# Kernel optimization log

Hardware: AMD Instinct MI355X
Metric: run time of the kernel (lower is better)

The kernel has to match this reference:

```python
import jax, jax.numpy as jnp
import numpy as np

N = 100000   # nodes
E = 800000   # edges
IN = 256     # input feature dim
H = 4        # heads per layer
D = 32       # per-head hidden dim (num_hidden)
SLOPE = 0.2  # leaky_relu negative slope


def setup_inputs() -> dict:
    key = jax.random.key(0)
    ks = jax.random.split(key, 8)
    s = 0.1  # weight scale for numerical stability
    x = jax.random.normal(ks[0], (N, IN), jnp.float32)
    edge_index = jax.random.randint(ks[1], (2, E), 0, N, dtype=jnp.int32)
    W0 = jax.random.normal(ks[2], (IN, H * D), jnp.float32) * s
    al0 = jax.random.normal(ks[3], (H, D), jnp.float32) * s
    ar0 = jax.random.normal(ks[4], (H, D), jnp.float32) * s
    W1 = jax.random.normal(ks[5], (H * D, H * D), jnp.float32) * s
    al1 = jax.random.normal(ks[6], (H, D), jnp.float32) * s
    ar1 = jax.random.normal(ks[7], (H, D), jnp.float32) * s
    return {"x": x, "edge_index": edge_index, "W0": W0, "al0": al0,
            "ar0": ar0, "W1": W1, "al1": al1, "ar1": ar1}


def _gat_layer(h, W, al, ar, src, dst, residual):
    """One GATConv: project, edge attention, dst-wise softmax, scatter-agg."""
    n = h.shape[0]
    feat = (h @ W).reshape(n, H, D)              # [N,H,D]
    el = jnp.einsum('nhd,hd->nh', feat, al)      # [N,H]
    er = jnp.einsum('nhd,hd->nh', feat, ar)      # [N,H]
    e = jax.nn.leaky_relu(el[src] + er[dst], SLOPE)   # raw scores [E,H]
    # edge softmax grouped by destination node (numerically stable)
    emax = jax.ops.segment_max(e, dst, num_segments=n)   # [N,H]
    eexp = jnp.exp(e - emax[dst])                          # [E,H]
    denom = jax.ops.segment_sum(eexp, dst, num_segments=n)  # [N,H]
    a = eexp / denom[dst]                                  # attention [E,H]
    msg = feat[src] * a[:, :, None]                        # [E,H,D]
    rst = jax.ops.segment_sum(msg, dst, num_segments=n)    # [N,H,D]
    if residual:
        rst = rst + h.reshape(n, H, D)  # identity residual (dims match)
    rst = jax.nn.elu(rst)               # activation
    return rst, a, e


def reference(x, edge_index, W0, al0, ar0, W1, al1, ar1):
    src, dst = edge_index[0], edge_index[1]
    # layer 0: no residual
    h1, a0, e0 = _gat_layer(x, W0, al0, ar0, src, dst, residual=False)
    atten0 = e0.mean(axis=-1)  # e_gat.flatten(1).mean(-1) -> [E]
    # layer 1: residual
    h2, a1, e1 = _gat_layer(h1.reshape(N, H * D), W1, al1, ar1, src, dst,
                            residual=True)
    atten1 = e1.mean(axis=-1)
    temp = h2.reshape(N, H * D)          # flattened node embeddings
    heads = tuple(h2[:, i] for i in range(H))  # per-head [N,D]
    return (temp,) + heads + (e1, atten0, atten1)
```

## Files before the change

### kernel.cpp

```cpp
#include <hip/hip_runtime.h>
#include <hip/hip_bf16.h>


typedef _Float16 f16;
typedef _Float16 f16x2 __attribute__((ext_vector_type(2)));
typedef _Float16 f16x8 __attribute__((ext_vector_type(8)));
typedef float f32x4 __attribute__((ext_vector_type(4)));

__global__ void wsplit2(const float* __restrict__ W0, const float* __restrict__ W1,
                        f16* __restrict__ Wth0, f16* __restrict__ Wtl0,
                        f16* __restrict__ Wth1, f16* __restrict__ Wtl1) {
    int i = blockIdx.x * blockDim.x + threadIdx.x;
    if (i < 256 * 128) {
        int k = i >> 7, c = i & 127;
        float v = W0[i];
        f16 h = (f16)v;
        Wth0[(size_t)c * 256 + k] = h;
        Wtl0[(size_t)c * 256 + k] = (f16)(v - (float)h);
    } else if (i < 256 * 128 + 128 * 128) {
        int j = i - 256 * 128;
        int k = j >> 7, c = j & 127;
        float v = W1[j];
        f16 h = (f16)v;
        Wth1[(size_t)c * 128 + k] = h;
        Wtl1[(size_t)c * 128 + k] = (f16)(v - (float)h);
    }
}

template <int AFP16>
__global__ __launch_bounds__(256, 2) void gemm_mfma(
        const void* __restrict__ Xv, const f16* __restrict__ Wth,
        const f16* __restrict__ Wtl, f16* __restrict__ Y16,
        const float* __restrict__ al, const float* __restrict__ ar,
        float* __restrict__ el_out, float* __restrict__ er_out,
        int nrows, int K) {
    constexpr int STR = 40;
    __shared__ f16 ash[128 * STR];
    __shared__ f16 asl[AFP16 ? 2 : 128 * STR];
    __shared__ f16 bsh[128 * STR];
    __shared__ f16 bsl[128 * STR];
    const int t    = threadIdx.x;
    const int wave = t >> 6;
    const int lane = t & 63;
    const int lr   = lane & 15;
    const int kg   = lane >> 4;
    const int row0 = blockIdx.x * 128;

    const int sr  = t >> 1;
    const int sko = (t & 1) * 16;
    const int ps  = ((sr & 7) << 4) | (sr >> 3);
    int gr = row0 + sr; if (gr >= nrows) gr = nrows - 1;

    f32x4 acc[2][8];
    #pragma unroll
    for (int i = 0; i < 2; ++i)
        #pragma unroll
        for (int j = 0; j < 8; ++j) acc[i][j] = (f32x4){0.f, 0.f, 0.f, 0.f};

    for (int k0 = 0; k0 < K; k0 += 32) {
        if constexpr (!AFP16) {
            const float* xp = (const float*)Xv + (size_t)gr * K + k0 + sko;
            float4 v0 = *(const float4*)(xp + 0);
            float4 v1 = *(const float4*)(xp + 4);
            float4 v2 = *(const float4*)(xp + 8);
            float4 v3 = *(const float4*)(xp + 12);
            float vv[16] = {v0.x, v0.y, v0.z, v0.w, v1.x, v1.y, v1.z, v1.w,
                            v2.x, v2.y, v2.z, v2.w, v3.x, v3.y, v3.z, v3.w};
            f16x8 H0, H1, L0, L1;
            #pragma unroll
            for (int i = 0; i < 8; ++i) {
                f16 h0 = (f16)vv[i];
                H0[i] = h0;
                L0[i] = (f16)(vv[i] - (float)h0);
                f16 h1 = (f16)vv[i + 8];
                H1[i] = h1;
                L1[i] = (f16)(vv[i + 8] - (float)h1);
            }
            *(f16x8*)&ash[sr * STR + sko]     = H0;
            *(f16x8*)&ash[sr * STR + sko + 8] = H1;
            *(f16x8*)&asl[sr * STR + sko]     = L0;
            *(f16x8*)&asl[sr * STR + sko + 8] = L1;
        } else {
            const f16* xp = (const f16*)Xv + (size_t)gr * K + k0 + sko;
            f16x8 a0 = *(const f16x8*)(xp);
            f16x8 a1 = *(const f16x8*)(xp + 8);
            *(f16x8*)&ash[sr * STR + sko]     = a0;
            *(f16x8*)&ash[sr * STR + sko + 8] = a1;
        }
        {
            const f16* bph = Wth + (size_t)sr * K + k0 + sko;
            const f16* bpl = Wtl + (size_t)sr * K + k0 + sko;
            f16x8 b0 = *(const f16x8*)(bph);
            f16x8 b1 = *(const f16x8*)(bph + 8);
            f16x8 b2 = *(const f16x8*)(bpl);
            f16x8 b3 = *(const f16x8*)(bpl + 8);
            *(f16x8*)&bsh[ps * STR + sko]     = b0;
            *(f16x8*)&bsh[ps * STR + sko + 8] = b1;
            *(f16x8*)&bsl[ps * STR + sko]     = b2;
            *(f16x8*)&bsl[ps * STR + sko + 8] = b3;
        }
        __syncthreads();

        const int arow = wave * 32 + lr;
        f16x8 ah0 = *(const f16x8*)&ash[arow * STR + kg * 8];
        f16x8 ah1 = *(const f16x8*)&ash[(arow + 16) * STR + kg * 8];
        f16x8 bh[8];
        #pragma unroll
        for (int cb = 0; cb < 8; ++cb)
            bh[cb] = *(const f16x8*)&bsh[(cb * 16 + lr) * STR + kg * 8];

        #pragma unroll
        for (int cb = 0; cb < 8; ++cb) {
            acc[0][cb] = __builtin_amdgcn_mfma_f32_16x16x32_f16(ah0, bh[cb], acc[0][cb], 0, 0, 0);
            acc[1][cb] = __builtin_amdgcn_mfma_f32_16x16x32_f16(ah1, bh[cb], acc[1][cb], 0, 0, 0);
        }
        if constexpr (!AFP16) {
            f16x8 al0_ = *(const f16x8*)&asl[arow * STR + kg * 8];
            f16x8 al1_ = *(const f16x8*)&asl[(arow + 16) * STR + kg * 8];
            #pragma unroll
            for (int cb = 0; cb < 8; ++cb) {
                acc[0][cb] = __builtin_amdgcn_mfma_f32_16x16x32_f16(al0_, bh[cb], acc[0][cb], 0, 0, 0);
                acc[1][cb] = __builtin_amdgcn_mfma_f32_16x16x32_f16(al1_, bh[cb], acc[1][cb], 0, 0, 0);
            }
        }
        #pragma unroll
        for (int cb = 0; cb < 8; ++cb) {
            f16x8 bl = *(const f16x8*)&bsl[(cb * 16 + lr) * STR + kg * 8];
            acc[0][cb] = __builtin_amdgcn_mfma_f32_16x16x32_f16(ah0, bl, acc[0][cb], 0, 0, 0);
            acc[1][cb] = __builtin_amdgcn_mfma_f32_16x16x32_f16(ah1, bl, acc[1][cb], 0, 0, 0);
        }
        __syncthreads();
    }

    const int hh = lr >> 2;
    const int co = (lr & 3) * 8;
    float alv[8], arv[8];
    #pragma unroll
    for (int j = 0; j < 8; ++j) {
        alv[j] = al[hh * 32 + co + j];
        arv[j] = ar[hh * 32 + co + j];
    }
    #pragma unroll
    for (int rb = 0; rb < 2; ++rb) {
        int rbase = row0 + wave * 32 + rb * 16 + kg * 4;
        #pragma unroll
        for (int r = 0; r < 4; ++r) {
            int grow = rbase + r;
            f16x8 hv;
            float sl_ = 0.0f, sr_ = 0.0f;
            #pragma unroll
            for (int cb = 0; cb < 8; ++cb) {
                float v = acc[rb][cb][r];
                hv[cb] = (f16)v;
                sl_ += v * alv[cb];
                sr_ += v * arv[cb];
            }
            sl_ += __shfl_xor(sl_, 1); sl_ += __shfl_xor(sl_, 2);
            sr_ += __shfl_xor(sr_, 1); sr_ += __shfl_xor(sr_, 2);
            if (grow < nrows) {
                *(f16x8*)(Y16 + (size_t)grow * 128 + lr * 8) = hv;
                if ((lane & 3) == 0) {
                    el_out[4 * (size_t)grow + hh] = sl_;
                    er_out[4 * (size_t)grow + hh] = sr_;
                }
            }
        }
    }
}

__global__ void count_deg(const int* __restrict__ dsts, int* __restrict__ deg, int E) {
    int e = blockIdx.x * blockDim.x + threadIdx.x;
    if (e < E) atomicAdd(&deg[dsts[e]], 1);
}

__global__ __launch_bounds__(256) void scan_block(const int* __restrict__ deg,
                                                  int* __restrict__ excl,
                                                  int* __restrict__ bsums, int n) {
    __shared__ int wsums[4];
    int t = threadIdx.x;
    int base = blockIdx.x * 1024;
    int idx = base + t * 4;
    int v[4];
    #pragma unroll
    for (int i = 0; i < 4; ++i) v[i] = (idx + i < n) ? deg[idx + i] : 0;
    int tsum = v[0] + v[1] + v[2] + v[3];
    int lane = t & 63, wid = t >> 6;
    int incl = tsum;
    #pragma unroll
    for (int off = 1; off < 64; off <<= 1) {
        int u = __shfl_up(incl, off, 64);
        if (lane >= off) incl += u;
    }
    if (lane == 63) wsums[wid] = incl;
    __syncthreads();
    if (t == 0) {
        int s = 0;
        #pragma unroll
        for (int w = 0; w < 4; ++w) { int x = wsums[w]; wsums[w] = s; s += x; }
    }
    __syncthreads();
    int ex = incl - tsum + wsums[wid];
    int run = ex;
    #pragma unroll
    for (int i = 0; i < 4; ++i) { if (idx + i < n) excl[idx + i] = run; run += v[i]; }
    if (t == 255) bsums[blockIdx.x] = ex + tsum;
}

__global__ __launch_bounds__(256) void scan_sums(int* __restrict__ bs, int nb) {
    __shared__ int wsums[4];
    int t = threadIdx.x;
    int v = (t < nb) ? bs[t] : 0;
    int lane = t & 63, wid = t >> 6;
    int incl = v;
    #pragma unroll
    for (int off = 1; off < 64; off <<= 1) {
        int u = __shfl_up(incl, off, 64);
        if (lane >= off) incl += u;
    }
    if (lane == 63) wsums[wid] = incl;
    __syncthreads();
    if (t == 0) {
        int s = 0;
        #pragma unroll
        for (int w = 0; w < 4; ++w) { int x = wsums[w]; wsums[w] = s; s += x; }
    }
    __syncthreads();
    if (t < nb) bs[t] = incl - v + wsums[wid];
}

__global__ void scan_finalize(int* __restrict__ row_off, const int* __restrict__ bsums,
                              int* __restrict__ cursor, int n) {
    int i = blockIdx.x * blockDim.x + threadIdx.x;
    if (i < n) {
        int v = row_off[i] + bsums[i >> 10];
        row_off[i] = v;
        cursor[i]  = v;
    }
}

__global__ void fill_csr_edge0(const int* __restrict__ srcs, const int* __restrict__ dsts,
                               int* __restrict__ cursor, int* __restrict__ csr_src,
                               const float* __restrict__ el, const float* __restrict__ er,
                               float* __restrict__ atten0, int E) {
    int e = blockIdx.x * blockDim.x + threadIdx.x;
    if (e >= E) return;
    int s = srcs[e], d = dsts[e];
    int p = atomicAdd(&cursor[d], 1);
    csr_src[p] = s;
    float4 elv = *(const float4*)(el + 4 * (size_t)s);
    float4 erv = *(const float4*)(er + 4 * (size_t)d);
    float v0 = elv.x + erv.x, v1 = elv.y + erv.y;
    float v2 = elv.z + erv.z, v3 = elv.w + erv.w;
    v0 = v0 > 0.0f ? v0 : 0.2f * v0;
    v1 = v1 > 0.0f ? v1 : 0.2f * v1;
    v2 = v2 > 0.0f ? v2 : 0.2f * v2;
    v3 = v3 > 0.0f ? v3 : 0.2f * v3;
    atten0[e] = (v0 + v1 + v2 + v3) * 0.25f;
}

__global__ void edge1_kernel(const int* __restrict__ srcs, const int* __restrict__ dsts,
                             const float* __restrict__ el, const float* __restrict__ er,
                             float* __restrict__ e1_out, float* __restrict__ atten1,
                             int E) {
    int e = blockIdx.x * blockDim.x + threadIdx.x;
    if (e >= E) return;
    int s = srcs[e], d = dsts[e];
    float4 elv = *(const float4*)(el + 4 * (size_t)s);
    float4 erv = *(const float4*)(er + 4 * (size_t)d);
    float v0 = elv.x + erv.x, v1 = elv.y + erv.y;
    float v2 = elv.z + erv.z, v3 = elv.w + erv.w;
    v0 = v0 > 0.0f ? v0 : 0.2f * v0;
    v1 = v1 > 0.0f ? v1 : 0.2f * v1;
    v2 = v2 > 0.0f ? v2 : 0.2f * v2;
    v3 = v3 > 0.0f ? v3 : 0.2f * v3;
    *(float4*)(e1_out + 4 * (size_t)e) = make_float4(v0, v1, v2, v3);
    atten1[e] = (v0 + v1 + v2 + v3) * 0.25f;
}

template <int LAYER>
__global__ __launch_bounds__(256) void aggregate(const int* __restrict__ row_off,
                                                 const int* __restrict__ deg,
                                                 const int* __restrict__ csr_src,
                                                 const float* __restrict__ el,
                                                 const float* __restrict__ er,
                                                 const f16* __restrict__ feat16,
                                                 const f16* __restrict__ resid16,
                                                 f16* __restrict__ out16,
                                                 float* __restrict__ out32,
                                                 float* __restrict__ heads,
                                                 int N) {
    int wave = (blockIdx.x * 256 + threadIdx.x) >> 6;
    if (wave >= N) return;
    int lane = threadIdx.x & 63;
    int q  = lane >> 4;
    int sc = lane & 15;
    int h  = sc >> 2;
    int start = row_off[wave];
    int dc    = deg[wave];
    float er_h = er[4 * (size_t)wave + h];

    float acc[8];
    #pragma unroll
    for (int j = 0; j < 8; ++j) acc[j] = 0.0f;
    float dh = 0.0f;

    for (int cs = 0; cs < dc; cs += 64) {
        int act = dc - cs; if (act > 64) act = 64;
        int sl = (lane < act) ? csr_src[start + cs + lane] : 0;
        int i = 0;
        for (; i + 8 <= act; i += 8) {
            int s0 = __shfl(sl, i + q);
            int s1 = __shfl(sl, i + 4 + q);
            float x0 = el[4 * (size_t)s0 + h] + er_h;
            float x1 = el[4 * (size_t)s1 + h] + er_h;
            x0 = x0 > 0.0f ? x0 : 0.2f * x0;
            x1 = x1 > 0.0f ? x1 : 0.2f * x1;
            float w0 = __expf(x0);
            float w1 = __expf(x1);
            f16x8 f0 = *(const f16x8*)(feat16 + 128 * (size_t)s0 + sc * 8);
            f16x8 f1 = *(const f16x8*)(feat16 + 128 * (size_t)s1 + sc * 8);
            #pragma unroll
            for (int j = 0; j < 8; ++j) acc[j] += w0 * (float)f0[j];
            #pragma unroll
            for (int j = 0; j < 8; ++j) acc[j] += w1 * (float)f1[j];
            dh += w0 + w1;
        }
        for (; i < act; i += 4) {
            int e = i + q;
            bool on = e < act;
            int s = __shfl(sl, on ? e : 0);
            float x = el[4 * (size_t)s + h] + er_h;
            x = x > 0.0f ? x : 0.2f * x;
            float w = on ? __expf(x) : 0.0f;
            f16x8 fv = *(const f16x8*)(feat16 + 128 * (size_t)s + sc * 8);
            #pragma unroll
            for (int j = 0; j < 8; ++j) acc[j] += w * (float)fv[j];
            dh += w;
        }
    }

    #pragma unroll
    for (int j = 0; j < 8; ++j) {
        acc[j] += __shfl_xor(acc[j], 16);
        acc[j] += __shfl_xor(acc[j], 32);
    }
    dh += __shfl_xor(dh, 16);
    dh += __shfl_xor(dh, 32);

    float inv = (dc > 0) ? 1.0f / dh : 0.0f;
    float ax = (q == 0) ? acc[0] : (q == 1) ? acc[2] : (q == 2) ? acc[4] : acc[6];
    float ay = (q == 0) ? acc[1] : (q == 1) ? acc[3] : (q == 2) ? acc[5] : acc[7];
    ax *= inv; ay *= inv;
    int c0 = sc * 8 + q * 2;
    size_t o = 128 * (size_t)wave + c0;
    if (LAYER == 1) {
        f16x2 rv = *(const f16x2*)(resid16 + o);
        ax += (float)rv[0]; ay += (float)rv[1];
    }
    ax = ax > 0.0f ? ax : __expf(ax) - 1.0f;
    ay = ay > 0.0f ? ay : __expf(ay) - 1.0f;
    if (LAYER == 0) {
        f16x2 hv; hv[0] = (f16)ax; hv[1] = (f16)ay;
        *(f16x2*)(out16 + o) = hv;
    } else {
        *(float2*)(out32 + o) = make_float2(ax, ay);
        *(float2*)(heads + (size_t)h * N * 32 + (size_t)wave * 32 + (c0 & 31)) =
            make_float2(ax, ay);
    }
}

extern "C" void kernel_launch(void* const* d_in, const int* in_sizes, int n_in,
                              void* d_out, int out_size, void* d_ws, size_t ws_size,
                              hipStream_t stream) {
    const float* x   = (const float*)d_in[0];
    const int*   ei  = (const int*)d_in[1];
    const float* W0  = (const float*)d_in[2];
    const float* al0 = (const float*)d_in[3];
    const float* ar0 = (const float*)d_in[4];
    const float* W1  = (const float*)d_in[5];
    const float* al1 = (const float*)d_in[6];
    const float* ar1 = (const float*)d_in[7];

    const int N = in_sizes[0] / 256;
    const int E = in_sizes[1] / 2;
    const size_t NF = (size_t)N * 128;

    const int* srcs = ei;
    const int* dsts = ei + E;

    float* out = (float*)d_out;
    f16*   f16ws  = (f16*)d_ws;
    f16*   feat16 = f16ws;
    f16*   h1_16  = feat16 + NF;
    float* el   = (float*)(h1_16 + NF);
    float* er   = el + (size_t)N * 4;
    f16*   wth0 = (f16*)(er + (size_t)N * 4);
    f16*   wtl0 = wth0 + (size_t)128 * 256;
    f16*   wth1 = wtl0 + (size_t)128 * 256;
    f16*   wtl1 = wth1 + (size_t)128 * 128;
    int*   ints    = (int*)(wtl1 + (size_t)128 * 128);
    int*   deg     = ints;
    int*   row_off = deg + N;
    int*   cursor  = row_off + N;
    int*   csr_src = cursor + N;
    int*   bsums   = csr_src + E;

    float* heads      = out + NF;
    float* e1_out     = out + 2 * NF;
    float* atten0_out = e1_out + (size_t)E * 4;
    float* atten1_out = atten0_out + E;

    const int wtot = 256 * 128 + 128 * 128;
    wsplit2<<<(wtot + 255) / 256, 256, 0, stream>>>(W0, W1, wth0, wtl0, wth1, wtl1);

    hipMemsetAsync(deg, 0, (size_t)N * sizeof(int), stream);
    count_deg<<<(E + 255) / 256, 256, 0, stream>>>(dsts, deg, E);
    int nb = (N + 1023) / 1024;
    scan_block<<<nb, 256, 0, stream>>>(deg, row_off, bsums, N);
    scan_sums<<<1, 256, 0, stream>>>(bsums, nb);
    scan_finalize<<<(N + 255) / 256, 256, 0, stream>>>(row_off, bsums, cursor, N);

    const int gemm_blocks = (N + 127) / 128;
    const int agg_blocks  = (N + 3) / 4;

    gemm_mfma<0><<<gemm_blocks, 256, 0, stream>>>(x, wth0, wtl0, feat16, al0, ar0,
                                                  el, er, N, 256);
    fill_csr_edge0<<<(E + 255) / 256, 256, 0, stream>>>(srcs, dsts, cursor, csr_src,
                                                        el, er, atten0_out, E);
    aggregate<0><<<agg_blocks, 256, 0, stream>>>(row_off, deg, csr_src, el, er,
                                                 feat16, nullptr, h1_16, nullptr,
                                                 nullptr, N);

    gemm_mfma<1><<<gemm_blocks, 256, 0, stream>>>(h1_16, wth1, wtl1, feat16, al1, ar1,
                                                  el, er, N, 128);
    edge1_kernel<<<(E + 255) / 256, 256, 0, stream>>>(srcs, dsts, el, er,
                                                      e1_out, atten1_out, E);
    aggregate<1><<<agg_blocks, 256, 0, stream>>>(row_off, deg, csr_src, el, er,
                                                 feat16, h1_16, nullptr, out,
                                                 heads, N);
}
```

Baseline: 443.5 us.

## Use direct global-to-LDS loads in GEMM, fuse prep kernels, nontemporal stores

The GEMM now stages A and B tiles with global_load_lds (direct global-to-LDS DMA) using XOR-swizzled layouts, and the fp32-to-fp16 hi/lo split of X moves from the staging phase to after the LDS read. The weight split and degree counting become one prep kernel, and the two scan-sums/finalize kernels become one kernel that reduces block sums itself. Output stores in the edge and aggregate kernels become nontemporal. These aim to cut register staging, launch count and cache pollution, at the cost of doing the split conversion redundantly per wave and carrying more LDS traffic for fp32 A.

```diff
diff --git a/kernel.cpp b/kernel.cpp
--- a/kernel.cpp
+++ b/kernel.cpp
@@ -5,11 +5,19 @@
 typedef _Float16 f16;
 typedef _Float16 f16x2 __attribute__((ext_vector_type(2)));
 typedef _Float16 f16x8 __attribute__((ext_vector_type(8)));
+typedef float f32x2 __attribute__((ext_vector_type(2)));
 typedef float f32x4 __attribute__((ext_vector_type(4)));
 
-__global__ void wsplit2(const float* __restrict__ W0, const float* __restrict__ W1,
-                        f16* __restrict__ Wth0, f16* __restrict__ Wtl0,
-                        f16* __restrict__ Wth1, f16* __restrict__ Wtl1) {
+__device__ __forceinline__ void gload16(const void* g, void* l) {
+    __builtin_amdgcn_global_load_lds(
+        (const __attribute__((address_space(1))) unsigned int*)g,
+        (__attribute__((address_space(3))) unsigned int*)l, 16, 0, 0);
+}
+
+__global__ void prep(const float* __restrict__ W0, const float* __restrict__ W1,
+                     f16* __restrict__ Wth0, f16* __restrict__ Wtl0,
+                     f16* __restrict__ Wth1, f16* __restrict__ Wtl1,
+                     const int* __restrict__ dsts, int* __restrict__ deg, int E) {
     int i = blockIdx.x * blockDim.x + threadIdx.x;
     if (i < 256 * 128) {
         int k = i >> 7, c = i & 127;
@@ -24,6 +32,9 @@
         f16 h = (f16)v;
         Wth1[(size_t)c * 128 + k] = h;
         Wtl1[(size_t)c * 128 + k] = (f16)(v - (float)h);
+    } else {
+        int e = i - (256 * 128 + 128 * 128);
+        if (e < E) atomicAdd(&deg[dsts[e]], 1);
     }
 }
 
@@ -34,11 +45,10 @@
         const float* __restrict__ al, const float* __restrict__ ar,
         float* __restrict__ el_out, float* __restrict__ er_out,
         int nrows, int K) {
-    constexpr int STR = 40;
-    __shared__ f16 ash[128 * STR];
-    __shared__ f16 asl[AFP16 ? 2 : 128 * STR];
-    __shared__ f16 bsh[128 * STR];
-    __shared__ f16 bsl[128 * STR];
+    __shared__ float As32[AFP16 ? 1 : 128 * 32];
+    __shared__ f16   As16[AFP16 ? 128 * 32 : 1];
+    __shared__ f16   Bh[128 * 32];
+    __shared__ f16   Bl[128 * 32];
     const int t    = threadIdx.x;
     const int wave = t >> 6;
     const int lane = t & 63;
@@ -46,11 +56,6 @@
     const int kg   = lane >> 4;
     const int row0 = blockIdx.x * 128;
 
-    const int sr  = t >> 1;
-    const int sko = (t & 1) * 16;
-    const int ps  = ((sr & 7) << 4) | (sr >> 3);
-    int gr = row0 + sr; if (gr >= nrows) gr = nrows - 1;
-
     f32x4 acc[2][8];
     #pragma unroll
     for (int i = 0; i < 2; ++i)
@@ -59,55 +64,59 @@
 
     for (int k0 = 0; k0 < K; k0 += 32) {
         if constexpr (!AFP16) {
-            const float* xp = (const float*)Xv + (size_t)gr * K + k0 + sko;
-            float4 v0 = *(const float4*)(xp + 0);
-            float4 v1 = *(const float4*)(xp + 4);
-            float4 v2 = *(const float4*)(xp + 8);
-            float4 v3 = *(const float4*)(xp + 12);
-            float vv[16] = {v0.x, v0.y, v0.z, v0.w, v1.x, v1.y, v1.z, v1.w,
-                            v2.x, v2.y, v2.z, v2.w, v3.x, v3.y, v3.z, v3.w};
-            f16x8 H0, H1, L0, L1;
+            #pragma unroll
+            for (int j = 0; j < 4; ++j) {
+                int G = t + 256 * j;
+                int row = G >> 3, slot = G & 7;
+                int g = slot ^ (row & 7);
+                int grow = row0 + row; if (grow >= nrows) grow = nrows - 1;
+                gload16((const float*)Xv + (size_t)grow * K + k0 + g * 4,
+                        &As32[G * 4]);
+            }
+        } else {
+            #pragma unroll
+            for (int j = 0; j < 2; ++j) {
+                int G = t + 256 * j;
+                int row = G >> 2, g4 = G & 3;
+                int grow = row0 + row; if (grow >= nrows) grow = nrows - 1;
+                gload16((const f16*)Xv + (size_t)grow * K + k0 + g4 * 8,
+                        &As16[G * 8]);
+            }
+        }
+        #pragma unroll
+        for (int j = 0; j < 2; ++j) {
+            int G = t + 256 * j;
+            int r = G >> 2, g4 = G & 3;
+            int p = ((r & 15) << 3) | (r >> 4);
+            gload16(Wth + (size_t)p * K + k0 + g4 * 8, &Bh[G * 8]);
+            gload16(Wtl + (size_t)p * K + k0 + g4 * 8, &Bl[G * 8]);
+        }
+        __syncthreads();
+
+        const int ar0_ = wave * 32 + lr;
+        f16x8 ah0, ah1, alo0, alo1;
+        if constexpr (!AFP16) {
+            int s0 = (2 * kg) ^ (lr & 7);
+            int s1 = (2 * kg + 1) ^ (lr & 7);
+            f32x4 u0 = *(const f32x4*)&As32[ar0_ * 32 + s0 * 4];
+            f32x4 u1 = *(const f32x4*)&As32[ar0_ * 32 + s1 * 4];
+            f32x4 v0 = *(const f32x4*)&As32[(ar0_ + 16) * 32 + s0 * 4];
+            f32x4 v1 = *(const f32x4*)&As32[(ar0_ + 16) * 32 + s1 * 4];
+            float a8[8] = {u0[0], u0[1], u0[2], u0[3], u1[0], u1[1], u1[2], u1[3]};
+            float b8[8] = {v0[0], v0[1], v0[2], v0[3], v1[0], v1[1], v1[2], v1[3]};
             #pragma unroll
             for (int i = 0; i < 8; ++i) {
-                f16 h0 = (f16)vv[i];
-                H0[i] = h0;
-                L0[i] = (f16)(vv[i] - (float)h0);
-                f16 h1 = (f16)vv[i + 8];
-                H1[i] = h1;
-                L1[i] = (f16)(vv[i + 8] - (float)h1);
-            }
-            *(f16x8*)&ash[sr * STR + sko]     = H0;
-            *(f16x8*)&ash[sr * STR + sko + 8] = H1;
-            *(f16x8*)&asl[sr * STR + sko]     = L0;
-            *(f16x8*)&asl[sr * STR + sko + 8] = L1;
+                f16 h0 = (f16)a8[i]; ah0[i] = h0; alo0[i] = (f16)(a8[i] - (float)h0);
+                f16 h1 = (f16)b8[i]; ah1[i] = h1; alo1[i] = (f16)(b8[i] - (float)h1);
+            }
         } else {
-            const f16* xp = (const f16*)Xv + (size_t)gr * K + k0 + sko;
-            f16x8 a0 = *(const f16x8*)(xp);
-            f16x8 a1 = *(const f16x8*)(xp + 8);
-            *(f16x8*)&ash[sr * STR + sko]     = a0;
-            *(f16x8*)&ash[sr * STR + sko + 8] = a1;
-        }
-        {
-            const f16* bph = Wth + (size_t)sr * K + k0 + sko;
-            const f16* bpl = Wtl + (size_t)sr * K + k0 + sko;
-            f16x8 b0 = *(const f16x8*)(bph);
-            f16x8 b1 = *(const f16x8*)(bph + 8);
-            f16x8 b2 = *(const f16x8*)(bpl);
-            f16x8 b3 = *(const f16x8*)(bpl + 8);
-            *(f16x8*)&bsh[ps * STR + sko]     = b0;
-            *(f16x8*)&bsh[ps * STR + sko + 8] = b1;
-            *(f16x8*)&bsl[ps * STR + sko]     = b2;
-            *(f16x8*)&bsl[ps * STR + sko + 8] = b3;
-        }
-        __syncthreads();
-
-        const int arow = wave * 32 + lr;
-        f16x8 ah0 = *(const f16x8*)&ash[arow * STR + kg * 8];
-        f16x8 ah1 = *(const f16x8*)&ash[(arow + 16) * STR + kg * 8];
+            ah0 = *(const f16x8*)&As16[ar0_ * 32 + kg * 8];
+            ah1 = *(const f16x8*)&As16[(ar0_ + 16) * 32 + kg * 8];
+        }
         f16x8 bh[8];
         #pragma unroll
         for (int cb = 0; cb < 8; ++cb)
-            bh[cb] = *(const f16x8*)&bsh[(cb * 16 + lr) * STR + kg * 8];
+            bh[cb] = *(const f16x8*)&Bh[(cb * 16 + lr) * 32 + kg * 8];
 
         #pragma unroll
         for (int cb = 0; cb < 8; ++cb) {
@@ -115,17 +124,15 @@
             acc[1][cb] = __builtin_amdgcn_mfma_f32_16x16x32_f16(ah1, bh[cb], acc[1][cb], 0, 0, 0);
         }
         if constexpr (!AFP16) {
-            f16x8 al0_ = *(const f16x8*)&asl[arow * STR + kg * 8];
-            f16x8 al1_ = *(const f16x8*)&asl[(arow + 16) * STR + kg * 8];
             #pragma unroll
             for (int cb = 0; cb < 8; ++cb) {
-                acc[0][cb] = __builtin_amdgcn_mfma_f32_16x16x32_f16(al0_, bh[cb], acc[0][cb], 0, 0, 0);
-                acc[1][cb] = __builtin_amdgcn_mfma_f32_16x16x32_f16(al1_, bh[cb], acc[1][cb], 0, 0, 0);
+                acc[0][cb] = __builtin_amdgcn_mfma_f32_16x16x32_f16(alo0, bh[cb], acc[0][cb], 0, 0, 0);
+                acc[1][cb] = __builtin_amdgcn_mfma_f32_16x16x32_f16(alo1, bh[cb], acc[1][cb], 0, 0, 0);
             }
         }
         #pragma unroll
         for (int cb = 0; cb < 8; ++cb) {
-            f16x8 bl = *(const f16x8*)&bsl[(cb * 16 + lr) * STR + kg * 8];
+            f16x8 bl = *(const f16x8*)&Bl[(cb * 16 + lr) * 32 + kg * 8];
             acc[0][cb] = __builtin_amdgcn_mfma_f32_16x16x32_f16(ah0, bl, acc[0][cb], 0, 0, 0);
             acc[1][cb] = __builtin_amdgcn_mfma_f32_16x16x32_f16(ah1, bl, acc[1][cb], 0, 0, 0);
         }
@@ -168,11 +175,6 @@
     }
 }
 
-__global__ void count_deg(const int* __restrict__ dsts, int* __restrict__ deg, int E) {
-    int e = blockIdx.x * blockDim.x + threadIdx.x;
-    if (e < E) atomicAdd(&deg[dsts[e]], 1);
-}
-
 __global__ __launch_bounds__(256) void scan_block(const int* __restrict__ deg,
                                                   int* __restrict__ excl,
                                                   int* __restrict__ bsums, int n) {
@@ -206,35 +208,33 @@
     if (t == 255) bsums[blockIdx.x] = ex + tsum;
 }
 
-__global__ __launch_bounds__(256) void scan_sums(int* __restrict__ bs, int nb) {
-    __shared__ int wsums[4];
+__global__ __launch_bounds__(256) void scan_fin(int* __restrict__ row_off,
+                                                const int* __restrict__ bsums,
+                                                int* __restrict__ cursor,
+                                                int n, int nb) {
+    __shared__ int spfx;
+    int b = blockIdx.x;
     int t = threadIdx.x;
-    int v = (t < nb) ? bs[t] : 0;
-    int lane = t & 63, wid = t >> 6;
-    int incl = v;
-    #pragma unroll
-    for (int off = 1; off < 64; off <<= 1) {
-        int u = __shfl_up(incl, off, 64);
-        if (lane >= off) incl += u;
-    }
-    if (lane == 63) wsums[wid] = incl;
+    if (t < 64) {
+        int v = 0;
+        if (t < b && t < nb) v = bsums[t];
+        int t2 = t + 64;
+        if (t2 < b && t2 < nb) v += bsums[t2];
+        #pragma unroll
+        for (int off = 32; off; off >>= 1) v += __shfl_xor(v, off, 64);
+        if (t == 0) spfx = v;
+    }
     __syncthreads();
-    if (t == 0) {
-        int s = 0;
-        #pragma unroll
-        for (int w = 0; w < 4; ++w) { int x = wsums[w]; wsums[w] = s; s += x; }
-    }
-    __syncthreads();
-    if (t < nb) bs[t] = incl - v + wsums[wid];
-}
-
-__global__ void scan_finalize(int* __restrict__ row_off, const int* __restrict__ bsums,
-                              int* __restrict__ cursor, int n) {
-    int i = blockIdx.x * blockDim.x + threadIdx.x;
-    if (i < n) {
-        int v = row_off[i] + bsums[i >> 10];
-        row_off[i] = v;
-        cursor[i]  = v;
+    int pfx = spfx;
+    int base = b * 1024 + t * 4;
+    #pragma unroll
+    for (int i2 = 0; i2 < 4; ++i2) {
+        int i = base + i2;
+        if (i < n) {
+            int v = row_off[i] + pfx;
+            row_off[i] = v;
+            cursor[i]  = v;
+        }
     }
 }
 
@@ -255,7 +255,7 @@
     v1 = v1 > 0.0f ? v1 : 0.2f * v1;
     v2 = v2 > 0.0f ? v2 : 0.2f * v2;
     v3 = v3 > 0.0f ? v3 : 0.2f * v3;
-    atten0[e] = (v0 + v1 + v2 + v3) * 0.25f;
+    __builtin_nontemporal_store((v0 + v1 + v2 + v3) * 0.25f, atten0 + e);
 }
 
 __global__ void edge1_kernel(const int* __restrict__ srcs, const int* __restrict__ dsts,
@@ -273,8 +273,9 @@
     v1 = v1 > 0.0f ? v1 : 0.2f * v1;
     v2 = v2 > 0.0f ? v2 : 0.2f * v2;
     v3 = v3 > 0.0f ? v3 : 0.2f * v3;
-    *(float4*)(e1_out + 4 * (size_t)e) = make_float4(v0, v1, v2, v3);
-    atten1[e] = (v0 + v1 + v2 + v3) * 0.25f;
+    __builtin_nontemporal_store((f32x4){v0, v1, v2, v3},
+                                (f32x4*)(e1_out + 4 * (size_t)e));
+    __builtin_nontemporal_store((v0 + v1 + v2 + v3) * 0.25f, atten1 + e);
 }
 
 template <int LAYER>
@@ -363,9 +364,10 @@
         f16x2 hv; hv[0] = (f16)ax; hv[1] = (f16)ay;
         *(f16x2*)(out16 + o) = hv;
     } else {
-        *(float2*)(out32 + o) = make_float2(ax, ay);
-        *(float2*)(heads + (size_t)h * N * 32 + (size_t)wave * 32 + (c0 & 31)) =
-            make_float2(ax, ay);
+        __builtin_nontemporal_store((f32x2){ax, ay}, (f32x2*)(out32 + o));
+        __builtin_nontemporal_store(
+            (f32x2){ax, ay},
+            (f32x2*)(heads + (size_t)h * N * 32 + (size_t)wave * 32 + (c0 & 31)));
     }
 }
 
@@ -410,15 +412,13 @@
     float* atten0_out = e1_out + (size_t)E * 4;
     float* atten1_out = atten0_out + E;
 
+    hipMemsetAsync(deg, 0, (size_t)N * sizeof(int), stream);
     const int wtot = 256 * 128 + 128 * 128;
-    wsplit2<<<(wtot + 255) / 256, 256, 0, stream>>>(W0, W1, wth0, wtl0, wth1, wtl1);
-
-    hipMemsetAsync(deg, 0, (size_t)N * sizeof(int), stream);
-    count_deg<<<(E + 255) / 256, 256, 0, stream>>>(dsts, deg, E);
+    prep<<<(wtot + E + 255) / 256, 256, 0, stream>>>(W0, W1, wth0, wtl0, wth1, wtl1,
+                                                     dsts, deg, E);
     int nb = (N + 1023) / 1024;
     scan_block<<<nb, 256, 0, stream>>>(deg, row_off, bsums, N);
-    scan_sums<<<1, 256, 0, stream>>>(bsums, nb);
-    scan_finalize<<<(N + 255) / 256, 256, 0, stream>>>(row_off, bsums, cursor, N);
+    scan_fin<<<nb, 256, 0, stream>>>(row_off, bsums, cursor, N, nb);
 
     const int gemm_blocks = (N + 127) / 128;
     const int agg_blocks  = (N + 3) / 4;
```

After: 427.0 us. -3.7%, faster.
